# Optimization experiments

Hardware: AMD Instinct MI355X
Metric: run time of the kernel (lower is better)

The kernel has to match this reference:

```python
import jax, jax.numpy as jnp
import numpy as np

# Camera model constants (expected-value camera: gain multiply + baseline offset)
GAIN = 2.0
BASELINE = 100.0

B, E = 32, 64          # frames, emitters per frame
H = W = 128            # image size
R = 13                 # PSF ROI (patch) size
D = 32                 # number of z slices in the spline table


def setup_inputs() -> dict:
    key = jax.random.key(0)
    k1, k2, k3, k4 = jax.random.split(key, 4)
    # subpixel emitter positions: x in [0,W), y in [0,H), z in voxel units [0, D-1)
    u = jax.random.uniform(k1, (B, E, 3), dtype=jnp.float32)
    xyz = u * jnp.array([W, H, D - 1], dtype=jnp.float32)
    n_photons = 1000.0 + 4000.0 * jax.random.uniform(k2, (B, E), dtype=jnp.float32)
    bg = 10.0 + 90.0 * jax.random.uniform(k3, (B, H, W), dtype=jnp.float32)
    # cubic-spline coefficient table: [z_slice, roi_y, roi_x, 4(dz),4(dy),4(dx)]
    coeff = 0.01 * jax.random.normal(k4, (D, R, R, 4, 4, 4), dtype=jnp.float32)
    return {"xyz": xyz, "n_photons": n_photons, "bg": bg, "coeff": coeff}


def reference(xyz, n_photons, bg, coeff):
    Bb, Hh, Ww = bg.shape
    Dd, Rr = coeff.shape[0], coeff.shape[1]
    half = Rr // 2
    pow4 = jnp.arange(4)

    def render_one(pos, nph):
        x, y, z = pos[0], pos[1], pos[2]
        xf, yf = jnp.floor(x), jnp.floor(y)
        dx, dy = x - xf, y - yf
        zc = jnp.clip(z, 0.0, Dd - 1.0 - 1e-6)
        zf = jnp.floor(zc)
        zi = zf.astype(jnp.int32)
        dz = zc - zf
        px = dx ** pow4  # [4]
        py = dy ** pow4
        pz = dz ** pow4
        c = coeff[zi]  # [R,R,4,4,4] gather of this emitter's z-slice
        patch = jnp.einsum('yxabc,a,b,c->yx', c, pz, py, px) * nph  # [R,R]
        r0 = yf.astype(jnp.int32) - half
        c0 = xf.astype(jnp.int32) - half
        rows = r0 + jnp.arange(Rr)
        cols = c0 + jnp.arange(Rr)
        img = jnp.zeros((Hh, Ww), patch.dtype)
        # irregular scatter-add of the PSF patch; OOB (incl. negative) dropped
        return img.at[rows[:, None], cols[None, :]].add(patch, mode='drop')

    imgs = jax.vmap(jax.vmap(render_one))(xyz, n_photons)  # [B,E,H,W]
    y = imgs + bg[:, None]          # add background per frame
    return y * GAIN + BASELINE      # camera gain
```

## Files before the change

kernel.cpp:

```cpp
#include <hip/hip_runtime.h>

constexpr int   B = 32, E = 64, H = 128, W = 128, R = 13, D = 32;
constexpr float GAIN = 2.0f, BASELINE = 100.0f;
constexpr int   HALF = R / 2;
constexpr int   PLANE = H * W;
constexpr int   PLANE4 = PLANE / 4;

__device__ __forceinline__ float pw(float v, int p) {
    float r = 1.0f;
    if (p >= 1) r = v;
    if (p >= 2) r *= v;
    if (p >= 3) r *= v;
    return r;
}

__global__ __launch_bounds__(256)
void stream_bg_kernel(const float* __restrict__ bg,
                      float* __restrict__ out)
{
    const int tid = threadIdx.x;
    const long long base4 = (long long)blockIdx.x * 1024;
    #pragma unroll
    for (int j = 0; j < 4; ++j) {
        const long long idx4 = base4 + j * 256 + tid;
        const int within4 = (int)(idx4 & (PLANE4 - 1));
        const int b       = (int)(idx4 >> 18);
        const float4 v = *(const float4*)(bg + ((size_t)b << 14) + ((size_t)within4 << 2));
        float4 o;
        o.x = v.x * GAIN + BASELINE;
        o.y = v.y * GAIN + BASELINE;
        o.z = v.z * GAIN + BASELINE;
        o.w = v.w * GAIN + BASELINE;
        *(float4*)(out + (idx4 << 2)) = o;
    }
}

__global__ __launch_bounds__(256)
void patch_kernel(const float* __restrict__ xyz,
                  const float* __restrict__ n_photons,
                  const float* __restrict__ bg,
                  const float* __restrict__ coeff,
                  float* __restrict__ out)
{
    const int be  = blockIdx.x;
    const int b   = be >> 6;
    const int tid = threadIdx.x;

    __shared__ float s_w[64];

    const float x = xyz[be * 3 + 0];
    const float y = xyz[be * 3 + 1];
    const float z = xyz[be * 3 + 2];
    const float nph = n_photons[be];

    const float xf = floorf(x), yf = floorf(y);
    const float dx = x - xf,   dy = y - yf;
    float zc = fminf(fmaxf(z, 0.0f), (float)(D - 1) - 1e-6f);
    const float zf = floorf(zc);
    const int   zi = (int)zf;
    const float dz = zc - zf;

    const int r0 = (int)yf - HALF;
    const int c0 = (int)xf - HALF;

    if (tid < 64) {
        const int a  = tid >> 4;
        const int bb = (tid >> 2) & 3;
        const int c  = tid & 3;
        s_w[tid] = pw(dz, a) * pw(dy, bb) * pw(dx, c);
    }
    __syncthreads();

    if (tid < R * R) {
        const int pr = tid / R;
        const int pc = tid - pr * R;

        const float* cp = coeff + (((size_t)zi * R + pr) * R + pc) * 64;
        float acc = 0.0f;
        #pragma unroll
        for (int k = 0; k < 64; k += 4) {
            const float4 cc = *(const float4*)(cp + k);
            acc += cc.x * s_w[k + 0];
            acc += cc.y * s_w[k + 1];
            acc += cc.z * s_w[k + 2];
            acc += cc.w * s_w[k + 3];
        }
        const float patch = acc * nph;

        int row = r0 + pr;  if (row < 0) row += H;
        int col = c0 + pc;  if (col < 0) col += W;
        if (row < H && col < W) {
            const size_t ppix = ((size_t)(row << 7)) + col;
            const float  bgv  = bg[((size_t)b << 14) + ppix];
            out[((size_t)be << 14) + ppix] = (bgv + patch) * GAIN + BASELINE;
        }
    }
}

extern "C" void kernel_launch(void* const* d_in, const int* in_sizes, int n_in,
                              void* d_out, int out_size, void* d_ws, size_t ws_size,
                              hipStream_t stream) {
    const float* xyz       = (const float*)d_in[0];
    const float* n_photons = (const float*)d_in[1];
    const float* bg        = (const float*)d_in[2];
    const float* coeff     = (const float*)d_in[3];
    float* out = (float*)d_out;

    stream_bg_kernel<<<dim3(8192), dim3(256), 0, stream>>>(bg, out);
    patch_kernel<<<dim3(B * E), dim3(256), 0, stream>>>(xyz, n_photons, bg, coeff, out);
}
```

Before: 162.6 us.

## Fuse background streaming and patch scatter into one quarter-plane kernel

Replaces the two-kernel scheme (full background write, then patch overwrite) with a single kernel where each block handles a 32-row quarter of one emitter's output plane. The block computes the spline patch in shared memory only when the patch overlaps its rows, then adds it while streaming the background, using nontemporal stores. This removes the second kernel launch and the extra read-modify-write of patch pixels. In exchange, blocks that need the patch synchronise before streaming.

```diff
diff --git a/kernel.cpp b/kernel.cpp
--- a/kernel.cpp
+++ b/kernel.cpp
@@ -3,8 +3,8 @@
 constexpr int   B = 32, E = 64, H = 128, W = 128, R = 13, D = 32;
 constexpr float GAIN = 2.0f, BASELINE = 100.0f;
 constexpr int   HALF = R / 2;
-constexpr int   PLANE = H * W;
-constexpr int   PLANE4 = PLANE / 4;
+
+typedef float f4_t __attribute__((ext_vector_type(4)));
 
 __device__ __forceinline__ float pw(float v, int p) {
     float r = 1.0f;
@@ -15,85 +15,96 @@
 }
 
 __global__ __launch_bounds__(256)
-void stream_bg_kernel(const float* __restrict__ bg,
-                      float* __restrict__ out)
-{
-    const int tid = threadIdx.x;
-    const long long base4 = (long long)blockIdx.x * 1024;
-    #pragma unroll
-    for (int j = 0; j < 4; ++j) {
-        const long long idx4 = base4 + j * 256 + tid;
-        const int within4 = (int)(idx4 & (PLANE4 - 1));
-        const int b       = (int)(idx4 >> 18);
-        const float4 v = *(const float4*)(bg + ((size_t)b << 14) + ((size_t)within4 << 2));
-        float4 o;
-        o.x = v.x * GAIN + BASELINE;
-        o.y = v.y * GAIN + BASELINE;
-        o.z = v.z * GAIN + BASELINE;
-        o.w = v.w * GAIN + BASELINE;
-        *(float4*)(out + (idx4 << 2)) = o;
-    }
-}
-
-__global__ __launch_bounds__(256)
-void patch_kernel(const float* __restrict__ xyz,
+void fused_kernel(const float* __restrict__ xyz,
                   const float* __restrict__ n_photons,
                   const float* __restrict__ bg,
                   const float* __restrict__ coeff,
                   float* __restrict__ out)
 {
-    const int be  = blockIdx.x;
+    const int bid = blockIdx.x;
+    const int q   = bid & 3;
+    const int be  = bid >> 2;
     const int b   = be >> 6;
     const int tid = threadIdx.x;
+    const int r_base = q << 5;
 
     __shared__ float s_w[64];
+    __shared__ float s_patch[R * R];
 
     const float x = xyz[be * 3 + 0];
     const float y = xyz[be * 3 + 1];
-    const float z = xyz[be * 3 + 2];
-    const float nph = n_photons[be];
 
     const float xf = floorf(x), yf = floorf(y);
-    const float dx = x - xf,   dy = y - yf;
-    float zc = fminf(fmaxf(z, 0.0f), (float)(D - 1) - 1e-6f);
-    const float zf = floorf(zc);
-    const int   zi = (int)zf;
-    const float dz = zc - zf;
-
     const int r0 = (int)yf - HALF;
     const int c0 = (int)xf - HALF;
 
-    if (tid < 64) {
-        const int a  = tid >> 4;
-        const int bb = (tid >> 2) & 3;
-        const int c  = tid & 3;
-        s_w[tid] = pw(dz, a) * pw(dy, bb) * pw(dx, c);
+    bool need;
+    {
+        const int lo = max(r0, 0), hi = min(r0 + R - 1, H - 1);
+        need = (lo <= r_base + 31) && (hi >= r_base);
+        if (r0 < 0 && r_base + 31 >= H + r0) need = true;
     }
-    __syncthreads();
 
-    if (tid < R * R) {
-        const int pr = tid / R;
-        const int pc = tid - pr * R;
+    if (need) {
+        const float z  = xyz[be * 3 + 2];
+        const float dx = x - xf, dy = y - yf;
+        float zc = fminf(fmaxf(z, 0.0f), (float)(D - 1) - 1e-6f);
+        const float zf = floorf(zc);
+        const int   zi = (int)zf;
+        const float dz = zc - zf;
+        if (tid < 64) {
+            const int a  = tid >> 4;
+            const int bb = (tid >> 2) & 3;
+            const int c  = tid & 3;
+            s_w[tid] = pw(dz, a) * pw(dy, bb) * pw(dx, c);
+        }
+        __syncthreads();
+        if (tid < R * R) {
+            const int pr = tid / R;
+            const int pc = tid - pr * R;
+            const float* cp = coeff + (((size_t)zi * R + pr) * R + pc) * 64;
+            float acc = 0.0f;
+            #pragma unroll
+            for (int k = 0; k < 64; k += 4) {
+                const f4_t cc = *(const f4_t*)(cp + k);
+                acc += cc.x * s_w[k + 0];
+                acc += cc.y * s_w[k + 1];
+                acc += cc.z * s_w[k + 2];
+                acc += cc.w * s_w[k + 3];
+            }
+            s_patch[tid] = acc * n_photons[be];
+        }
+        __syncthreads();
+    }
 
-        const float* cp = coeff + (((size_t)zi * R + pr) * R + pc) * 64;
-        float acc = 0.0f;
-        #pragma unroll
-        for (int k = 0; k < 64; k += 4) {
-            const float4 cc = *(const float4*)(cp + k);
-            acc += cc.x * s_w[k + 0];
-            acc += cc.y * s_w[k + 1];
-            acc += cc.z * s_w[k + 2];
-            acc += cc.w * s_w[k + 3];
+    const f4_t* bgp  = (const f4_t*)(bg  + ((size_t)b  << 14)) + (q << 10);
+    f4_t*       outp = (f4_t*)      (out + ((size_t)be << 14)) + (q << 10);
+
+    #pragma unroll
+    for (int j = 0; j < 4; ++j) {
+        const int f = (j << 8) + tid;
+        f4_t v = bgp[f];
+        if (need) {
+            const int row = r_base + (f >> 5);
+            int pr = row - r0;
+            if ((unsigned)pr >= (unsigned)R) pr = row - r0 - H;
+            if ((unsigned)pr < (unsigned)R) {
+                const float* prow = s_patch + pr * R;
+                const int cb = (f & 31) << 2;
+                #pragma unroll
+                for (int cmp = 0; cmp < 4; ++cmp) {
+                    int pc = cb + cmp - c0;
+                    if ((unsigned)pc >= (unsigned)R) pc = cb + cmp - c0 - W;
+                    if ((unsigned)pc < (unsigned)R) v[cmp] += prow[pc];
+                }
+            }
         }
-        const float patch = acc * nph;
-
-        int row = r0 + pr;  if (row < 0) row += H;
-        int col = c0 + pc;  if (col < 0) col += W;
-        if (row < H && col < W) {
-            const size_t ppix = ((size_t)(row << 7)) + col;
-            const float  bgv  = bg[((size_t)b << 14) + ppix];
-            out[((size_t)be << 14) + ppix] = (bgv + patch) * GAIN + BASELINE;
-        }
+        f4_t o;
+        o.x = v.x * GAIN + BASELINE;
+        o.y = v.y * GAIN + BASELINE;
+        o.z = v.z * GAIN + BASELINE;
+        o.w = v.w * GAIN + BASELINE;
+        __builtin_nontemporal_store(o, outp + f);
     }
 }
 
@@ -106,6 +117,6 @@
     const float* coeff     = (const float*)d_in[3];
     float* out = (float*)d_out;
 
-    stream_bg_kernel<<<dim3(8192), dim3(256), 0, stream>>>(bg, out);
-    patch_kernel<<<dim3(B * E), dim3(256), 0, stream>>>(xyz, n_photons, bg, coeff, out);
+    fused_kernel<<<dim3(B * E * 4), dim3(256), 0, stream>>>(
+        xyz, n_photons, bg, coeff, out);
 }
```

Measured after the change: 166.3 us. +2.3%, slower.
